# Performance work log

Measured on AMD Instinct MI355X. Metric: run time of the kernel, lower is better.

The kernel has to match this reference:

```python
import jax, jax.numpy as jnp
import numpy as np

LOGZERO = -1e10
BLANK, EOS = 0, 2
B, T, O = 8, 500, 10000
W = 8          # beam width -> n_bh = B*W hypotheses
SNUM = 200     # CTC pre-scoring label count


def setup_inputs() -> dict:
    key = jax.random.key(0)
    k1, k2, k3, k4, k5, k6 = jax.random.split(key, 6)
    n_bh = B * W
    # label log-posteriors (B, T, O)
    x = jax.nn.log_softmax(jax.random.normal(k1, (B, T, O), jnp.float32), axis=-1)
    xlens = jax.random.randint(k2, (B,), T // 2, T + 1).astype(jnp.int32)
    last_ids = jax.random.randint(k3, (n_bh,), 0, O).astype(jnp.int32)
    # unique scoring ids per hypothesis (pre-selected labels)
    scoring_ids = jax.vmap(lambda k: jax.random.permutation(k, O)[:SNUM])(
        jax.random.split(k4, n_bh)).astype(jnp.int32)
    r_prev = jax.random.normal(k5, (T, 2, n_bh), jnp.float32) - 5.0
    s_prev = jax.random.normal(k6, (n_bh, O), jnp.float32) * 0.1
    return dict(x=x, r_prev=r_prev, s_prev=s_prev, xlens=xlens,
                last_ids=last_ids, scoring_ids=scoring_ids, output_length=10)


def _forward(x, r_prev, s_prev, xlens, last_ids, scoring_ids, output_length):
    n_bh = last_ids.shape[0]
    n_hyps = n_bh // B
    snum = scoring_ids.shape[1]

    # ---- __init__: mask frames t >= xlens[b]: logzero everywhere, 0 at blank ----
    tmask = jnp.arange(T)[None, :] >= xlens[:, None]                    # (B,T)
    x = jnp.where(tmask[:, :, None], LOGZERO, x)
    x = x.at[:, :, BLANK].set(jnp.where(tmask, 0.0, x[:, :, BLANK]))
    xn = jnp.transpose(x, (1, 0, 2))                                    # (T,B,O)
    xb = jnp.broadcast_to(xn[:, :, BLANK][:, :, None], xn.shape)        # (T,B,O)
    xs = jnp.stack([xn, xb])                                            # (2,T,B,O)
    end_frames = xlens - 1

    b_of_hyp = jnp.arange(n_bh) // n_hyps                               # (n_bh,)
    # scoring_idmap: (n_bh, O), position of each label in scoring list, -1 if absent
    idmap = jnp.full((n_bh, O), -1, jnp.int32).at[
        jnp.arange(n_bh)[:, None], scoring_ids].set(
        jnp.broadcast_to(jnp.arange(snum, dtype=jnp.int32)[None, :], (n_bh, snum)))
    # gather scored labels: (2,T,n_bh,snum)
    x_ = xs[:, :, b_of_hyp[:, None], scoring_ids]

    r_sum = jax.scipy.special.logsumexp(r_prev, axis=1)                 # (T,n_bh)
    pos = idmap[jnp.arange(n_bh), last_ids]                             # (n_bh,)
    hit = (jnp.arange(snum)[None, :] == pos[:, None]) & (pos[:, None] >= 0)
    # log_phi: r_sum, except r_prev[:,1] where next label == last label
    log_phi = jnp.where(hit[None], r_prev[:, 1, :, None], r_sum[:, :, None])  # (T,n_bh,snum)

    start = max(int(output_length), 1)

    r0 = jnp.full((2, n_bh, snum), LOGZERO, x.dtype)
    if output_length == 0:
        r0 = r0.at[0].set(x_[0, 0])

    def step(rp, inp):
        phi_tm1, x_t = inp                                              # (n_bh,snum),(2,n_bh,snum)
        rn = jnp.logaddexp(rp[0], phi_tm1) + x_t[0]
        rb = jnp.logaddexp(rp[0], rp[1]) + x_t[1]
        rt = jnp.stack([rn, rb])
        return rt, rt

    _, r_scan = jax.lax.scan(step, r0,
                             (log_phi[start - 1:T - 1],
                              jnp.moveaxis(x_[:, start:T], 1, 0)))       # (T-start,2,n_bh,snum)
    r_pre = jnp.full((start, 2, n_bh, snum), LOGZERO, x.dtype)
    if output_length == 0:
        r_pre = r_pre.at[0, 0].set(x_[0, 0])
    r = jnp.concatenate([r_pre, r_scan], axis=0)                        # (T,2,n_bh,snum)

    # log_psi over scored labels
    log_phi_x = jnp.concatenate([log_phi[:1], log_phi[:-1]], axis=0) + x_[0]   # (T,n_bh,snum)
    psi_stack = jnp.concatenate([log_phi_x[start:T], r[start - 1, 0][None]], axis=0)
    log_psi_ = jax.scipy.special.logsumexp(psi_stack, axis=0)           # (n_bh,snum)

    log_psi = jnp.full((n_bh, O), LOGZERO, x.dtype).at[
        jnp.arange(n_bh)[:, None], scoring_ids].set(log_psi_)
    eos_score = r_sum[end_frames[b_of_hyp], jnp.arange(n_bh)]
    log_psi = log_psi.at[:, EOS].set(eos_score)
    log_psi = log_psi.at[:, BLANK].set(LOGZERO)
    return log_psi - s_prev                                             # (n_bh, O)


def reference(x, r_prev, s_prev, xlens, last_ids, scoring_ids, output_length):
    return _forward(x, r_prev, s_prev, xlens, last_ids, scoring_ids, output_length)
```

## Files before the change

kernel.cpp:

```cpp
#include <hip/hip_runtime.h>

#define LOGZERO -10000000000.0f

constexpr int Bc    = 8;
constexpr int Tc    = 500;
constexpr int Oc    = 10000;
constexpr int NBH   = 64;
constexpr int NHYP  = 8;
constexpr int SNUM  = 200;
constexpr int BLANK = 0;
constexpr int EOSID = 2;

constexpr int TC     = 4;
constexpr int NCHUNK = (Tc + TC - 1) / TC;
constexpr int NP     = 7;

__device__ __forceinline__ float logaddexp_f(float a, float b) {
    float m = fmaxf(a, b);
    return m + log1pf(expf(-fabsf(a - b)));
}

__global__ __launch_bounds__(256) void ctc_score_kernel(
    const float* __restrict__ x,
    const float* __restrict__ r_prev,
    const int*   __restrict__ xlens,
    const int*   __restrict__ last_ids,
    const int*   __restrict__ scoring_ids,
    const int*   __restrict__ olen_p,
    float*       __restrict__ acc_out)
{
    const int blk = blockIdx.x;
    const int b   = blk / NCHUNK;
    const int c   = blk % NCHUNK;
    const int t0  = c * TC;

    const int ol    = olen_p[0];
    const int start = (ol > 1) ? ol : 1;
    const int tlo   = (ol == 0) ? 0 : start;
    int xlen = xlens[b];
    if (xlen > Tc) xlen = Tc;
    const int lo = (t0 > tlo) ? t0 : tlo;
    const int hi = ((t0 + TC) < xlen) ? (t0 + TC) : xlen;
    if (lo >= hi) return;

    __shared__ __align__(16) float xrow[Oc];
    __shared__ float pno[NHYP];
    __shared__ float phit[NHYP];

    const int tid = threadIdx.x;

    int   sid[NP];
    int   jj[NP];
    bool  hit[NP];
    float acc[NP];
#pragma unroll
    for (int i = 0; i < NP; ++i) {
        acc[i] = 0.0f;
        int p = tid + i * 256;
        if (p < NHYP * SNUM) {
            int j = p / SNUM;
            int k = p - j * SNUM;
            int h = b * NHYP + j;
            int s = scoring_ids[h * SNUM + k];
            sid[i] = s;
            jj[i]  = j;
            hit[i] = (s == last_ids[h]);
        } else {
            sid[i] = 0; jj[i] = 0; hit[i] = false;
        }
    }

    for (int t = lo; t < hi; ++t) {
        const float4* row4 = (const float4*)(x + (size_t)(b * Tc + t) * Oc);
        float4* x4 = (float4*)xrow;
        for (int idx = tid; idx < Oc / 4; idx += 256) {
            x4[idx] = row4[idx];
        }
        if (tid < NHYP && t > 0) {
            int h = b * NHYP + tid;
            float r0 = r_prev[(size_t)(t - 1) * (2 * NBH) + h];
            float r1 = r_prev[(size_t)(t - 1) * (2 * NBH) + NBH + h];
            phit[tid] = r1;
            pno[tid]  = logaddexp_f(r0, r1);
        }
        __syncthreads();

#pragma unroll
        for (int i = 0; i < NP; ++i) {
            int p = tid + i * 256;
            if (p < NHYP * SNUM) {
                float ph = (t == 0) ? 0.0f : (hit[i] ? phit[jj[i]] : pno[jj[i]]);
                acc[i] += expf(ph + xrow[sid[i]]);
            }
        }
        __syncthreads();
    }

#pragma unroll
    for (int i = 0; i < NP; ++i) {
        int p = tid + i * 256;
        if (p < NHYP * SNUM && acc[i] != 0.0f) {
            int j = jj[i];
            int k = p - j * SNUM;
            int h = b * NHYP + j;
            atomicAdd(&acc_out[h * SNUM + k], acc[i]);
        }
    }
}

__global__ __launch_bounds__(256) void ctc_finalize_kernel(
    const float* __restrict__ r_prev,
    const float* __restrict__ s_prev,
    const int*   __restrict__ xlens,
    const int*   __restrict__ scoring_ids,
    const float* __restrict__ acc_in,
    float*       __restrict__ out)
{
    const int h   = blockIdx.x;
    const int b   = h / NHYP;
    const int tid = threadIdx.x;

    const int end = xlens[b] - 1;
    const float r0 = r_prev[(size_t)end * (2 * NBH) + h];
    const float r1 = r_prev[(size_t)end * (2 * NBH) + NBH + h];
    const float eos = logaddexp_f(r0, r1);

    const float4* sp4  = (const float4*)(s_prev + (size_t)h * Oc);
    float4*       out4 = (float4*)(out + (size_t)h * Oc);
    for (int idx = tid; idx < Oc / 4; idx += 256) {
        float4 s = sp4[idx];
        int o = idx * 4;
        float4 v;
        v.x = ((o + 0 == EOSID) ? eos : LOGZERO) - s.x;
        v.y = ((o + 1 == EOSID) ? eos : LOGZERO) - s.y;
        v.z = ((o + 2 == EOSID) ? eos : LOGZERO) - s.z;
        v.w = ((o + 3 == EOSID) ? eos : LOGZERO) - s.w;
        out4[idx] = v;
    }
    __syncthreads();

    if (tid < SNUM) {
        int o = scoring_ids[h * SNUM + tid];
        if (o != BLANK && o != EOSID) {
            float sum = acc_in[h * SNUM + tid];
            sum = fmaxf(sum, 1e-37f);
            float psi = logf(sum);
            out[(size_t)h * Oc + o] = psi - s_prev[(size_t)h * Oc + o];
        }
    }
}

extern "C" void kernel_launch(void* const* d_in, const int* in_sizes, int n_in,
                              void* d_out, int out_size, void* d_ws, size_t ws_size,
                              hipStream_t stream) {
    const float* x           = (const float*)d_in[0];
    const float* r_prev      = (const float*)d_in[1];
    const float* s_prev      = (const float*)d_in[2];
    const int*   xlens       = (const int*)d_in[3];
    const int*   last_ids    = (const int*)d_in[4];
    const int*   scoring_ids = (const int*)d_in[5];
    const int*   olen        = (const int*)d_in[6];
    float* out = (float*)d_out;
    float* acc = (float*)d_ws;

    hipMemsetAsync(acc, 0, NBH * SNUM * sizeof(float), stream);
    ctc_score_kernel<<<Bc * NCHUNK, 256, 0, stream>>>(
        x, r_prev, xlens, last_ids, scoring_ids, olen, acc);
    ctc_finalize_kernel<<<NBH, 256, 0, stream>>>(
        r_prev, s_prev, xlens, scoring_ids, acc, out);
}
```

Measured before the change: 239.9 us.

## Merge dense output fill into score kernel and batch row loads into registers

The dense fill of the output (EOS score and LOGZERO minus s_prev) now runs as extra blocks inside the scoring kernel, so it overlaps with the scoring work. The finalize kernel is reduced to a small scatter of the scored labels. Block indexing now interleaves batches across chunks. Per-chunk prefix values (r_prev logaddexp) are computed once up front instead of once per time step. Each x row is loaded into registers in one unrolled batch before being written to shared memory, which raises memory-level parallelism at some cost in registers.

Measured after the change: 258.6 us. 1.08x slower.

```diff
diff --git a/kernel.cpp b/kernel.cpp
--- a/kernel.cpp
+++ b/kernel.cpp
@@ -13,26 +13,57 @@
 
 constexpr int TC     = 4;
 constexpr int NCHUNK = (Tc + TC - 1) / TC;
+constexpr int NSCORE = Bc * NCHUNK;
 constexpr int NP     = 7;
+constexpr int NV4    = Oc / 4;
+constexpr int FULLI  = NV4 / 256;
+constexpr int REMT   = NV4 - FULLI * 256;
 
 __device__ __forceinline__ float logaddexp_f(float a, float b) {
     float m = fmaxf(a, b);
     return m + log1pf(expf(-fabsf(a - b)));
 }
 
-__global__ __launch_bounds__(256) void ctc_score_kernel(
+__global__ __launch_bounds__(256) void ctc_main_kernel(
     const float* __restrict__ x,
     const float* __restrict__ r_prev,
+    const float* __restrict__ s_prev,
     const int*   __restrict__ xlens,
     const int*   __restrict__ last_ids,
     const int*   __restrict__ scoring_ids,
     const int*   __restrict__ olen_p,
-    float*       __restrict__ acc_out)
+    float*       __restrict__ acc_out,
+    float*       __restrict__ out)
 {
     const int blk = blockIdx.x;
-    const int b   = blk / NCHUNK;
-    const int c   = blk % NCHUNK;
-    const int t0  = c * TC;
+    const int tid = threadIdx.x;
+
+    if (blk >= NSCORE) {
+        const int h = blk - NSCORE;
+        const int b = h >> 3;
+        const int end = xlens[b] - 1;
+        const float r0 = r_prev[(size_t)end * (2 * NBH) + h];
+        const float r1 = r_prev[(size_t)end * (2 * NBH) + NBH + h];
+        const float eos = logaddexp_f(r0, r1);
+
+        const float4* sp4  = (const float4*)(s_prev + (size_t)h * Oc);
+        float4*       out4 = (float4*)(out + (size_t)h * Oc);
+        for (int idx = tid; idx < NV4; idx += 256) {
+            float4 s = sp4[idx];
+            int o = idx * 4;
+            float4 v;
+            v.x = ((o + 0 == EOSID) ? eos : LOGZERO) - s.x;
+            v.y = ((o + 1 == EOSID) ? eos : LOGZERO) - s.y;
+            v.z = ((o + 2 == EOSID) ? eos : LOGZERO) - s.z;
+            v.w = ((o + 3 == EOSID) ? eos : LOGZERO) - s.w;
+            out4[idx] = v;
+        }
+        return;
+    }
+
+    const int c  = blk >> 3;
+    const int b  = blk & 7;
+    const int t0 = c * TC;
 
     const int ol    = olen_p[0];
     const int start = (ol > 1) ? ol : 1;
@@ -42,12 +73,27 @@
     const int lo = (t0 > tlo) ? t0 : tlo;
     const int hi = ((t0 + TC) < xlen) ? (t0 + TC) : xlen;
     if (lo >= hi) return;
+    const int nt = hi - lo;
 
     __shared__ __align__(16) float xrow[Oc];
-    __shared__ float pno[NHYP];
-    __shared__ float phit[NHYP];
+    __shared__ float pnoL[TC][NHYP];
+    __shared__ float phitL[TC][NHYP];
 
-    const int tid = threadIdx.x;
+    if (tid < nt * NHYP) {
+        const int ti = tid >> 3;
+        const int j  = tid & 7;
+        const int t  = lo + ti;
+        if (t == 0) {
+            pnoL[ti][j]  = 0.0f;
+            phitL[ti][j] = 0.0f;
+        } else {
+            const int h = b * NHYP + j;
+            const float r0 = r_prev[(size_t)(t - 1) * (2 * NBH) + h];
+            const float r1 = r_prev[(size_t)(t - 1) * (2 * NBH) + NBH + h];
+            phitL[ti][j] = r1;
+            pnoL[ti][j]  = logaddexp_f(r0, r1);
+        }
+    }
 
     int   sid[NP];
     int   jj[NP];
@@ -70,26 +116,23 @@
         }
     }
 
-    for (int t = lo; t < hi; ++t) {
+    for (int t = lo, ti = 0; t < hi; ++t, ++ti) {
         const float4* row4 = (const float4*)(x + (size_t)(b * Tc + t) * Oc);
         float4* x4 = (float4*)xrow;
-        for (int idx = tid; idx < Oc / 4; idx += 256) {
-            x4[idx] = row4[idx];
-        }
-        if (tid < NHYP && t > 0) {
-            int h = b * NHYP + tid;
-            float r0 = r_prev[(size_t)(t - 1) * (2 * NBH) + h];
-            float r1 = r_prev[(size_t)(t - 1) * (2 * NBH) + NBH + h];
-            phit[tid] = r1;
-            pno[tid]  = logaddexp_f(r0, r1);
-        }
+        float4 buf[FULLI + 1];
+#pragma unroll
+        for (int i = 0; i < FULLI; ++i) buf[i] = row4[tid + i * 256];
+        if (tid < REMT) buf[FULLI] = row4[tid + FULLI * 256];
+#pragma unroll
+        for (int i = 0; i < FULLI; ++i) x4[tid + i * 256] = buf[i];
+        if (tid < REMT) x4[tid + FULLI * 256] = buf[FULLI];
         __syncthreads();
 
 #pragma unroll
         for (int i = 0; i < NP; ++i) {
             int p = tid + i * 256;
             if (p < NHYP * SNUM) {
-                float ph = (t == 0) ? 0.0f : (hit[i] ? phit[jj[i]] : pno[jj[i]]);
+                float ph = hit[i] ? phitL[ti][jj[i]] : pnoL[ti][jj[i]];
                 acc[i] += expf(ph + xrow[sid[i]]);
             }
         }
@@ -108,37 +151,14 @@
     }
 }
 
-__global__ __launch_bounds__(256) void ctc_finalize_kernel(
-    const float* __restrict__ r_prev,
+__global__ __launch_bounds__(256) void ctc_scatter_kernel(
     const float* __restrict__ s_prev,
-    const int*   __restrict__ xlens,
     const int*   __restrict__ scoring_ids,
     const float* __restrict__ acc_in,
     float*       __restrict__ out)
 {
     const int h   = blockIdx.x;
-    const int b   = h / NHYP;
     const int tid = threadIdx.x;
-
-    const int end = xlens[b] - 1;
-    const float r0 = r_prev[(size_t)end * (2 * NBH) + h];
-    const float r1 = r_prev[(size_t)end * (2 * NBH) + NBH + h];
-    const float eos = logaddexp_f(r0, r1);
-
-    const float4* sp4  = (const float4*)(s_prev + (size_t)h * Oc);
-    float4*       out4 = (float4*)(out + (size_t)h * Oc);
-    for (int idx = tid; idx < Oc / 4; idx += 256) {
-        float4 s = sp4[idx];
-        int o = idx * 4;
-        float4 v;
-        v.x = ((o + 0 == EOSID) ? eos : LOGZERO) - s.x;
-        v.y = ((o + 1 == EOSID) ? eos : LOGZERO) - s.y;
-        v.z = ((o + 2 == EOSID) ? eos : LOGZERO) - s.z;
-        v.w = ((o + 3 == EOSID) ? eos : LOGZERO) - s.w;
-        out4[idx] = v;
-    }
-    __syncthreads();
-
     if (tid < SNUM) {
         int o = scoring_ids[h * SNUM + tid];
         if (o != BLANK && o != EOSID) {
@@ -164,8 +184,8 @@
     float* acc = (float*)d_ws;
 
     hipMemsetAsync(acc, 0, NBH * SNUM * sizeof(float), stream);
-    ctc_score_kernel<<<Bc * NCHUNK, 256, 0, stream>>>(
-        x, r_prev, xlens, last_ids, scoring_ids, olen, acc);
-    ctc_finalize_kernel<<<NBH, 256, 0, stream>>>(
-        r_prev, s_prev, xlens, scoring_ids, acc, out);
+    ctc_main_kernel<<<NSCORE + NBH, 256, 0, stream>>>(
+        x, r_prev, s_prev, xlens, last_ids, scoring_ids, olen, acc, out);
+    ctc_scatter_kernel<<<NBH, 256, 0, stream>>>(
+        s_prev, scoring_ids, acc, out);
 }
```
